# Kernel tuning notes

Measured on AMD Instinct MI355X. Metric: run time of the kernel, lower is better.

## Reference

```python
import jax, jax.numpy as jnp
import numpy as np


def _lstm_cell(x, h, c, Wih, Whh, bih, bhh):
    # torch.nn.LSTMCell: gates ordered (input, forget, cell, output)
    g = x @ Wih.T + h @ Whh.T + bih + bhh
    i, f, gg, o = jnp.split(g, 4, axis=-1)
    c2 = jax.nn.sigmoid(f) * c + jax.nn.sigmoid(i) * jnp.tanh(gg)
    h2 = jax.nn.sigmoid(o) * jnp.tanh(c2)
    return h2, c2


def setup_inputs() -> dict:
    key = jax.random.key(0)
    T, B, S, D = 64, 16, 128, 512
    ks = jax.random.split(key, 10)
    sc = 0.04  # ~ 1/sqrt(D) init scale
    z2 = jnp.zeros((B, D), jnp.float32)
    return {
        "emb_utts": jax.random.normal(ks[0], (T, B, D), jnp.float32),
        "M": jax.random.normal(ks[1], (B, S, D), jnp.float32),
        "hr0": z2, "cr0": z2, "hw0": z2, "cw0": z2,
        "Wih_r": jax.random.normal(ks[2], (4 * D, D), jnp.float32) * sc,
        "Whh_r": jax.random.normal(ks[3], (4 * D, D), jnp.float32) * sc,
        "bih_r": jnp.zeros((4 * D,), jnp.float32),
        "bhh_r": jnp.zeros((4 * D,), jnp.float32),
        "Wih_w": jax.random.normal(ks[4], (4 * D, D), jnp.float32) * sc,
        "Whh_w": jax.random.normal(ks[5], (4 * D, D), jnp.float32) * sc,
        "bih_w": jnp.zeros((4 * D,), jnp.float32),
        "bhh_w": jnp.zeros((4 * D,), jnp.float32),
        "Wc": jax.random.normal(ks[6], (D, 2 * D), jnp.float32) * sc,
        "bc": jnp.zeros((D,), jnp.float32),
    }


def reference(emb_utts, M, hr0, cr0, hw0, cw0,
              Wih_r, Whh_r, bih_r, bhh_r,
              Wih_w, Whh_w, bih_w, bhh_w, Wc, bc):
    def step(carry, w):
        hr, cr, hw, cw, Mc = carry
        # read LSTM (dropout is identity in eval)
        hr, cr = _lstm_cell(w, hr, cr, Wih_r, Whh_r, bih_r, bhh_r)
        # attention over memory
        sim = jnp.einsum('bd,bsd->bs', hr, Mc)
        z = jax.nn.softmax(sim, axis=-1)
        m = jnp.einsum('bs,bsd->bd', z, Mc)
        # compose + write LSTM
        comp = jnp.concatenate([hr, m], axis=-1) @ Wc.T + bc
        hw, cw = _lstm_cell(comp, hw, cw, Wih_w, Whh_w, bih_w, bhh_w)
        # memory update, faithful to source: M_new = (1 - z) * (M + hw)
        erase = 1.0 - z[:, :, None]
        Mc = erase * (Mc + hw[:, None, :])
        return (hr, cr, hw, cw, Mc), hw

    (hr, cr, hw, cw, Mf), outputs = jax.lax.scan(
        step, (hr0, cr0, hw0, cw0, M), emb_utts)
    return outputs, hr, cr, hw, cw, Mf
```

## Files before the change

kernel.cpp:

```cpp
#include <hip/hip_runtime.h>
#include <math.h>

#define TT 64
#define BB 16
#define SS 128
#define DD 512
#define NBLK 256
#define NTH 256
#define NSHARD 8
#define SHSTRIDE 64
#define BD (BB*DD)
#define OUT_HR   (TT*BD)
#define OUT_CR   (OUT_HR + BD)
#define OUT_HW   (OUT_CR + BD)
#define OUT_CW   (OUT_HW + BD)
#define OUT_MF   (OUT_CW + BD)
#define MAGIC 0x13579BDFu

#define HRR_OFF 0
#define HWR_OFF 532480
#define MR_OFF  1064960
#define SP_OFF  1589248
#define GE_OFF  1622016

#define OFF_WHR  0
#define OFF_WHW  4672
#define OFF_WFH  9344
#define OFF_WFM  14016
#define OFF_ABUF 18688
#define OFF_ML   28160
#define OFF_PRED 32256
#define OFF_GFB  36480
#define OFF_GFT  36608
#define OFF_ZL   36736
#define OFF_BFL  36992
#define OFF_SMW  37000
#define LDS_FLOATS 37008
#define LDS_BYTES  (LDS_FLOATS*4)
#define KH_W 292
#define KH_A 592

#define COLC(c) (((c) >> 1) * DD + dr0 + ((c) & 1))

__device__ __forceinline__ float sigf(float x) { return 1.f / (1.f + __expf(-x)); }

__device__ __forceinline__ void stg(float* p, float v) {
  __hip_atomic_store(p, v, __ATOMIC_RELAXED, __HIP_MEMORY_SCOPE_AGENT);
}
__device__ __forceinline__ float ldga(const float* p) {
  return __hip_atomic_load(p, __ATOMIC_RELAXED, __HIP_MEMORY_SCOPE_AGENT);
}

__device__ __forceinline__ void barrive(unsigned* cnt, unsigned& ep, int shard) {
  __syncthreads();
  if (threadIdx.x == 0) {
    ++ep;
    asm volatile("s_waitcnt vmcnt(0)" ::: "memory");
    __hip_atomic_fetch_add(cnt + shard * SHSTRIDE, 1u, __ATOMIC_RELAXED,
                           __HIP_MEMORY_SCOPE_AGENT);
  }
}
__device__ __forceinline__ void bwait(unsigned* cnt, unsigned ep) {
  if (threadIdx.x == 0) {
    const unsigned target = ep * (unsigned)NBLK;
    for (;;) {
      unsigned s = 0;
#pragma unroll
      for (int k = 0; k < NSHARD; ++k)
        s += __hip_atomic_load(cnt + k * SHSTRIDE, __ATOMIC_RELAXED,
                               __HIP_MEMORY_SCOPE_AGENT);
      if (s >= target) break;
      __builtin_amdgcn_s_sleep(1);
    }
  }
  __syncthreads();
}
__device__ __forceinline__ void lbar(unsigned* cnt, unsigned& ep, int shard) {
  barrive(cnt, ep, shard);
  bwait(cnt, ep);
}

__device__ __forceinline__ float dotf4(const float* __restrict__ a,
                                       const float* __restrict__ b, int n4) {
  const float4* a4 = (const float4*)a;
  const float4* b4 = (const float4*)b;
  float4 s = make_float4(0.f, 0.f, 0.f, 0.f);
#pragma unroll 8
  for (int k = 0; k < n4; ++k) {
    float4 x = a4[k], y = b4[k];
    s.x = fmaf(x.x, y.x, s.x); s.y = fmaf(x.y, y.y, s.y);
    s.z = fmaf(x.z, y.z, s.z); s.w = fmaf(x.w, y.w, s.w);
  }
  return (s.x + s.y) + (s.z + s.w);
}

__device__ __forceinline__ void dot_pass8(const float* __restrict__ A,
                                          const float* __restrict__ W,
                                          float* __restrict__ pout)
{
  float acc[8] = {0.f,0.f,0.f,0.f,0.f,0.f,0.f,0.f};
#pragma unroll
  for (int j = 0; j < 8; ++j) {
    float4 a4 = *(const float4*)(A + j*4);
#pragma unroll
    for (int c = 0; c < 8; ++c) {
      float4 w4 = *(const float4*)(W + c*36 + j*4);
      acc[c] = fmaf(a4.x, w4.x, acc[c]); acc[c] = fmaf(a4.y, w4.y, acc[c]);
      acc[c] = fmaf(a4.z, w4.z, acc[c]); acc[c] = fmaf(a4.w, w4.w, acc[c]);
    }
  }
  *(float4*)(pout)   = make_float4(acc[0],acc[1],acc[2],acc[3]);
  *(float4*)(pout+4) = make_float4(acc[4],acc[5],acc[6],acc[7]);
}

__device__ __forceinline__ void dot_pass8g(const float* __restrict__ ag,
                                           const float* __restrict__ Wb,
                                           int khq,
                                           float* __restrict__ pout)
{
  float acc[8] = {0.f,0.f,0.f,0.f,0.f,0.f,0.f,0.f};
#pragma unroll
  for (int jj = 0; jj < 2; ++jj) {
    const float* Wt = Wb + (khq*2 + jj)*KH_W;
#pragma unroll
    for (int j = 0; j < 8; ++j) {
      float4 a4 = *(const float4*)(ag + jj*32 + j*4);
#pragma unroll
      for (int c = 0; c < 8; ++c) {
        float4 w4 = *(const float4*)(Wt + c*36 + j*4);
        acc[c] = fmaf(a4.x, w4.x, acc[c]); acc[c] = fmaf(a4.y, w4.y, acc[c]);
        acc[c] = fmaf(a4.z, w4.z, acc[c]); acc[c] = fmaf(a4.w, w4.w, acc[c]);
      }
    }
  }
  *(float4*)(pout)   = make_float4(acc[0],acc[1],acc[2],acc[3]);
  *(float4*)(pout+4) = make_float4(acc[4],acc[5],acc[6],acc[7]);
}

__global__ void __launch_bounds__(NTH) memnet(
    const float* __restrict__ emb, const float* __restrict__ M_in,
    const float* __restrict__ hr0, const float* __restrict__ cr0,
    const float* __restrict__ hw0, const float* __restrict__ cw0,
    const float* __restrict__ Wih_r, const float* __restrict__ Whh_r,
    const float* __restrict__ bih_r, const float* __restrict__ bhh_r,
    const float* __restrict__ Wih_w, const float* __restrict__ Whh_w,
    const float* __restrict__ bih_w, const float* __restrict__ bhh_w,
    const float* __restrict__ Wc, const float* __restrict__ bc,
    float* __restrict__ out,
    unsigned* flagp, unsigned* cntp, float* __restrict__ wsf)
{
  extern __shared__ float L[];
  const int tid = threadIdx.x;
  const int bid = blockIdx.x;
  const int shard = bid & (NSHARD - 1);

  const int mb  = bid & 15;
  const int mdh = bid >> 4;
  const int dr0 = 2 * bid;

  float* hrr = wsf + HRR_OFF;
  float* hwr = wsf + HWR_OFF;
  float* mr  = wsf + MR_OFF;
  float* sp  = wsf + SP_OFF;
  float* gE  = wsf + GE_OFF + bid * (TT * 128);

  if (bid == 0) {
    if (tid == 0) {
#pragma unroll
      for (int k = 0; k < NSHARD; ++k)
        __hip_atomic_store(cntp + k * SHSTRIDE, 0u, __ATOMIC_RELAXED,
                           __HIP_MEMORY_SCOPE_AGENT);
      asm volatile("s_waitcnt vmcnt(0)" ::: "memory");
      __hip_atomic_store(flagp, MAGIC, __ATOMIC_RELAXED, __HIP_MEMORY_SCOPE_AGENT);
    }
  } else if (tid == 0) {
    while (__hip_atomic_load(flagp, __ATOMIC_RELAXED, __HIP_MEMORY_SCOPE_AGENT) != MAGIC) {}
  }
  __syncthreads();
  unsigned ep = 0;

  float cr = 0.f, cw = 0.f;
  if (tid >= 128 && tid < 160) {
    const int t = tid - 128, b = t & 15, dl = t >> 4;
    cr = cr0[b * DD + dr0 + dl];
    cw = cw0[b * DD + dr0 + dl];
  }

  {
    float* wih = L + OFF_ABUF;
#pragma unroll
    for (int c = 0; c < 8; ++c)
      ((float2*)(wih + c * DD))[tid] = ((const float2*)(Wih_w + COLC(c) * DD))[tid];
  }
  __syncthreads();
  {
    const float* wih = L + OFF_ABUF;
    float4 acc[8];
#pragma unroll
    for (int c = 0; c < 8; ++c) acc[c] = make_float4(0.f,0.f,0.f,0.f);
    const int k0 = tid * 4;
    for (int cc = 0; cc < DD; ++cc) {
      float4 wc4 = *(const float4*)(Wc + cc * 1024 + k0);
#pragma unroll
      for (int c = 0; c < 8; ++c) {
        const float wv = wih[c * DD + cc];
        acc[c].x = fmaf(wv, wc4.x, acc[c].x); acc[c].y = fmaf(wv, wc4.y, acc[c].y);
        acc[c].z = fmaf(wv, wc4.z, acc[c].z); acc[c].w = fmaf(wv, wc4.w, acc[c].w);
      }
    }
    const int kk = k0 & 511, kh = kk >> 5, jf = kk & 31;
    float* Tb = L + ((k0 < 512) ? OFF_WFH : OFF_WFM);
#pragma unroll
    for (int c = 0; c < 8; ++c)
      *(float4*)(Tb + kh*KH_W + c*36 + jf) = acc[c];
    if (tid < 8) {
      float s = 0.f;
      for (int cc = 0; cc < DD; ++cc) s = fmaf(wih[tid * DD + cc], bc[cc], s);
      L[OFF_BFL + tid] = s + bih_w[COLC(tid)] + bhh_w[COLC(tid)];
    }
  }
  __syncthreads();
  {
    const int c = tid >> 5, r = tid & 31;
    const int kk = r * 16, kh = kk >> 5, jb = (r & 1) * 16;
#pragma unroll
    for (int set = 0; set < 2; ++set) {
      const float* Wsrc = set ? Whh_w : Whh_r;
      float* dst = L + (set ? OFF_WHW : OFF_WHR) + kh*KH_W + c*36 + jb;
      const float* src = Wsrc + COLC(c) * DD + kk;
#pragma unroll
      for (int u = 0; u < 4; ++u)
        *(float4*)(dst + u*4) = *(const float4*)(src + u*4);
    }
  }
  {
    const int d_l = tid >> 3, sq = tid & 7;
    const int d = mdh * 32 + d_l;
#pragma unroll 4
    for (int j = 0; j < 16; ++j) {
      const int s = sq * 16 + j;
      L[OFF_ML + d_l * 128 + s] = M_in[(mb * SS + s) * DD + d];
    }
  }
  {
    const int tH = tid >> 7, b = (tid >> 3) & 15, c = tid & 7;
    const int col = COLC(c);
    const float bias = bih_r[col] + bhh_r[col];
    const float* wrow = Wih_r + col * DD;
    for (int t = tH * 32; t < tH * 32 + 32; ++t) {
      gE[t * 128 + b * 8 + c] = dotf4(emb + (t * BB + b) * DD, wrow, DD / 4) + bias;
    }
  }
  __syncthreads();
  {
#pragma unroll
    for (int j = 0; j < 8; ++j) {
      const int idx = j * 256 + tid;
      const int b = idx >> 7, k4 = idx & 127;
      const int kh = k4 >> 3, jf = (k4 & 7) * 4;
      float4 v = ((const float4*)hr0)[idx];
      *(float4*)(L + OFF_ABUF + kh*KH_A + b*36 + jf) = v;
    }
  }
  __syncthreads();
  {
    const int kh = tid >> 4, b = tid & 15;
    dot_pass8(L + OFF_ABUF + kh*KH_A + b*36, L + OFF_WHR + kh*KH_W,
              L + OFF_PRED + kh*132 + b*8);
  }
  __syncthreads();
  if (tid < 128) {
    float s = 0.f;
#pragma unroll
    for (int k2 = 0; k2 < 16; ++k2) s += L[OFF_PRED + k2*132 + tid];
    L[OFF_GFT + tid] = s;
  }
  __syncthreads();
  if (tid >= 128 && tid < 160) {
    const int t = tid - 128, b = t & 15, dl = t >> 4;
    float g[4];
#pragma unroll
    for (int q = 0; q < 4; ++q) {
      const int bc = b * 8 + q * 2 + dl;
      g[q] = L[OFF_GFT + bc] + gE[0 * 128 + bc];
    }
    cr = sigf(g[1]) * cr + sigf(g[0]) * tanhf(g[2]);
    const float h2 = sigf(g[3]) * tanhf(cr);
    stg(hrr + 1 * BD + b * DD + dr0 + dl, h2);
  }
  lbar(cntp, ep, shard);
  {
    const float* src = hrr + 1 * BD;
#pragma unroll
    for (int j = 0; j < 8; ++j) {
      const int idx = j * 256 + tid;
      const int b = idx >> 7, k4 = idx & 127;
      const int kh = k4 >> 3, jf = (k4 & 7) * 4;
      float4 v = ((const float4*)src)[idx];
      *(float4*)(L + OFF_ABUF + kh*KH_A + b*36 + jf) = v;
    }
  }
  __syncthreads();

  for (int i = 0; i < TT; ++i) {
    const int ii = i + 1;
    float* zold = L + OFF_ZL + ((i & 1) ^ 1) * 128;
    float* znew = L + OFF_ZL + (i & 1) * 128;

    {
      const int d_l = tid >> 3, sq = tid & 7;
      const float* Mrow = L + OFF_ML + d_l * 128;
      const float hrv = L[OFF_ABUF + mdh*KH_A + mb*36 + d_l];
#pragma unroll
      for (int j = 0; j < 4; ++j) {
        const int s4 = sq * 16 + j * 4;
        float4 M4 = *(const float4*)(Mrow + s4);
        float4 s;
        s.x = hrv * M4.x; s.y = hrv * M4.y; s.z = hrv * M4.z; s.w = hrv * M4.w;
        *(float4*)(L + OFF_PRED + d_l*132 + s4) = s;
      }
    }
    __syncthreads();
    if (tid < SS) {
      float v = 0.f;
#pragma unroll
      for (int dl2 = 0; dl2 < 32; ++dl2) v += L[OFF_PRED + dl2*132 + tid];
      stg(sp + (mb * 16 + mdh) * SS + tid, v);
    }
    barrive(cntp, ep, shard);

    if (ii < TT) {
      {
        const int kh = tid >> 4, b = tid & 15;
        dot_pass8(L + OFF_ABUF + kh*KH_A + b*36, L + OFF_WHR + kh*KH_W,
                  L + OFF_PRED + kh*132 + b*8);
      }
      __syncthreads();
      if (tid < 128) {
        float s = 0.f;
#pragma unroll
        for (int k2 = 0; k2 < 16; ++k2) s += L[OFF_PRED + k2*132 + tid];
        L[OFF_GFT + tid] = s;
      }
      __syncthreads();
      if (tid >= 128 && tid < 160) {
        const int t = tid - 128, b = t & 15, dl = t >> 4;
        float g[4];
#pragma unroll
        for (int q = 0; q < 4; ++q) {
          const int bc = b * 8 + q * 2 + dl;
          g[q] = L[OFF_GFT + bc] + gE[ii * 128 + bc];
        }
        cr = sigf(g[1]) * cr + sigf(g[0]) * tanhf(g[2]);
        const float h2 = sigf(g[3]) * tanhf(cr);
        stg(hrr + (ii + 1) * BD + b * DD + dr0 + dl, h2);
        if (ii == TT - 1) {
          out[OUT_HR + b * DD + dr0 + dl] = h2;
          out[OUT_CR + b * DD + dr0 + dl] = cr;
        }
      }
    }
    bwait(cntp, ep);

    float vsum = 0.f;
    if (tid < SS) {
#pragma unroll
      for (int j = 0; j < 16; ++j) vsum += ldga(sp + (mb * 16 + j) * SS + tid);
    } else if (i > 0) {
      const int t = tid - 128, k0 = t * 4;
      const float4 hw4 = *(const float4*)(hwr + i * BD + mb * DD + k0);
      const float4 a4  = *(const float4*)(L + OFF_ABUF + (k0 >> 5)*KH_A + mb*36 + (k0 & 31));
      float p = a4.x * hw4.x;
      p = fmaf(a4.y, hw4.y, p); p = fmaf(a4.z, hw4.z, p); p = fmaf(a4.w, hw4.w, p);
      for (int off = 32; off > 0; off >>= 1) p += __shfl_xor(p, off);
      if ((tid & 63) == 0) L[OFF_SMW + 6 + ((tid >> 6) & 1)] = p;
    }
    __syncthreads();
    if (tid < SS) {
      float v = vsum;
      if (i > 0) {
        const float hrdot = L[OFF_SMW + 6] + L[OFF_SMW + 7];
        v = (1.f - zold[tid]) * (v + hrdot);
      }
      float wm = v;
      for (int off = 32; off > 0; off >>= 1) wm = fmaxf(wm, __shfl_xor(wm, off));
      if ((tid & 63) == 0) L[OFF_SMW + (tid >> 6)] = wm;
      vsum = v;
    }
    __syncthreads();
    if (tid < SS) {
      const float gmax = fmaxf(L[OFF_SMW], L[OFF_SMW + 1]);
      const float e = __expf(vsum - gmax);
      float sm = e;
      for (int off = 32; off > 0; off >>= 1) sm += __shfl_xor(sm, off);
      if ((tid & 63) == 0) L[OFF_SMW + 2 + (tid >> 6)] = sm;
      vsum = e;
    }
    __syncthreads();
    if (tid < SS) znew[tid] = vsum / (L[OFF_SMW + 2] + L[OFF_SMW + 3]);
    __syncthreads();
    {
      const int d_l = tid >> 3, sq = tid & 7;
      float* Mrow = L + OFF_ML + d_l * 128;
      float mv = 0.f;
      if (i > 0) {
        const float hwv = hwr[i * BD + mb * DD + mdh * 32 + d_l];
#pragma unroll
        for (int j = 0; j < 4; ++j) {
          const int s4 = sq * 16 + j * 4;
          float4 M4  = *(float4*)(Mrow + s4);
          float4 zo4 = *(const float4*)(zold + s4);
          float4 zn4 = *(const float4*)(znew + s4);
          M4.x = (1.f - zo4.x) * (M4.x + hwv);
          M4.y = (1.f - zo4.y) * (M4.y + hwv);
          M4.z = (1.f - zo4.z) * (M4.z + hwv);
          M4.w = (1.f - zo4.w) * (M4.w + hwv);
          *(float4*)(Mrow + s4) = M4;
          mv = fmaf(zn4.x, M4.x, mv); mv = fmaf(zn4.y, M4.y, mv);
          mv = fmaf(zn4.z, M4.z, mv); mv = fmaf(zn4.w, M4.w, mv);
        }
      } else {
#pragma unroll
        for (int j = 0; j < 4; ++j) {
          const int s4 = sq * 16 + j * 4;
          float4 M4  = *(const float4*)(Mrow + s4);
          float4 zn4 = *(const float4*)(znew + s4);
          mv = fmaf(zn4.x, M4.x, mv); mv = fmaf(zn4.y, M4.y, mv);
          mv = fmaf(zn4.z, M4.z, mv); mv = fmaf(zn4.w, M4.w, mv);
        }
      }
      L[OFF_PRED + d_l * 8 + sq] = mv;
    }
    __syncthreads();
    if (tid < 32) {
      float mv = 0.f;
#pragma unroll
      for (int j = 0; j < 8; ++j) mv += L[OFF_PRED + tid * 8 + j];
      stg(mr + i * BD + mb * DD + mdh * 32 + tid, mv);
    }
    barrive(cntp, ep, shard);

    {
      const int kh = tid >> 4, b = tid & 15;
      dot_pass8(L + OFF_ABUF + kh*KH_A + b*36, L + OFF_WFH + kh*KH_W,
                L + OFF_PRED + 2112 + kh*132 + b*8);
    }
    bwait(cntp, ep);

    if (tid < 128) {
      float s = 0.f;
#pragma unroll
      for (int k2 = 0; k2 < 16; ++k2) s += L[OFF_PRED + 2112 + k2*132 + tid];
      L[OFF_GFB + tid] = s;
    }
    {
      const int src = tid >> 7, khq = (tid >> 4) & 7, b = tid & 15;
      const float* ag;
      const float* Wb;
      if (src == 0) { ag = mr + i * BD + b * DD + khq * 64; Wb = L + OFF_WFM; }
      else {
        const float* hwsrc = (i == 0) ? hw0 : (hwr + i * BD);
        ag = hwsrc + b * DD + khq * 64; Wb = L + OFF_WHW;
      }
      dot_pass8g(ag, Wb, khq, L + OFF_PRED + (src * 8 + khq) * 132 + b * 8);
    }
    __syncthreads();
    if (tid < 128) {
      float s = 0.f;
#pragma unroll
      for (int k2 = 0; k2 < 16; ++k2) s += L[OFF_PRED + k2*132 + tid];
      L[OFF_GFT + tid] = s;
    }
    __syncthreads();
    if (tid >= 128 && tid < 160) {
      const int t = tid - 128, b = t & 15, dl = t >> 4;
      float g[4];
#pragma unroll
      for (int q = 0; q < 4; ++q) {
        const int c = q * 2 + dl, bc = b * 8 + c;
        g[q] = L[OFF_GFB + bc] + L[OFF_GFT + bc] + L[OFF_BFL + c];
      }
      cw = sigf(g[1]) * cw + sigf(g[0]) * tanhf(g[2]);
      const float h2 = sigf(g[3]) * tanhf(cw);
      const int d = dr0 + dl;
      stg(hwr + (i + 1) * BD + b * DD + d, h2);
      out[i * BD + b * DD + d] = h2;
      if (i == TT - 1) {
        out[OUT_HW + b * DD + d] = h2;
        out[OUT_CW + b * DD + d] = cw;
      }
    }
    if (i < TT - 1) {
      const float* src = hrr + (i + 2) * BD;
#pragma unroll
      for (int j = 0; j < 8; ++j) {
        const int idx = j * 256 + tid;
        const int b = idx >> 7, k4 = idx & 127;
        const int kh = k4 >> 3, jf = (k4 & 7) * 4;
        float4 v = ((const float4*)src)[idx];
        *(float4*)(L + OFF_ABUF + kh*KH_A + b*36 + jf) = v;
      }
    }
    __syncthreads();
  }

  lbar(cntp, ep, shard);

  {
    const int d_l = tid >> 3, sq = tid & 7;
    const int d = mdh * 32 + d_l;
    const float hwv = hwr[TT * BD + mb * DD + d];
    const float* zfin = L + OFF_ZL + ((TT - 1) & 1) * 128;
#pragma unroll 4
    for (int j = 0; j < 16; ++j) {
      const int s = sq * 16 + j;
      const float nv = (1.f - zfin[s]) * (L[OFF_ML + d_l * 128 + s] + hwv);
      out[OUT_MF + (mb * SS + s) * DD + d] = nv;
    }
  }
}

extern "C" void kernel_launch(void* const* d_in, const int* in_sizes, int n_in,
                              void* d_out, int out_size, void* d_ws, size_t ws_size,
                              hipStream_t stream) {
  (void)in_sizes; (void)n_in; (void)out_size; (void)ws_size;
  const float* emb   = (const float*)d_in[0];
  const float* M_in  = (const float*)d_in[1];
  const float* hr0   = (const float*)d_in[2];
  const float* cr0   = (const float*)d_in[3];
  const float* hw0   = (const float*)d_in[4];
  const float* cw0   = (const float*)d_in[5];
  const float* Wih_r = (const float*)d_in[6];
  const float* Whh_r = (const float*)d_in[7];
  const float* bih_r = (const float*)d_in[8];
  const float* bhh_r = (const float*)d_in[9];
  const float* Wih_w = (const float*)d_in[10];
  const float* Whh_w = (const float*)d_in[11];
  const float* bih_w = (const float*)d_in[12];
  const float* bhh_w = (const float*)d_in[13];
  const float* Wc    = (const float*)d_in[14];
  const float* bc    = (const float*)d_in[15];
  float* out = (float*)d_out;

  char* wsb = (char*)d_ws;
  unsigned* flagp = (unsigned*)wsb;
  unsigned* cntp  = (unsigned*)(wsb + 1024);
  float* wsf = (float*)(wsb + 4096);

  static int attr_set = -1;
  (void)attr_set;
  hipFuncSetAttribute((const void*)memnet,
                      hipFuncAttributeMaxDynamicSharedMemorySize, LDS_BYTES);

  hipLaunchKernelGGL(memnet, dim3(NBLK), dim3(NTH), LDS_BYTES, stream,
                     emb, M_in, hr0, cr0, hw0, cw0,
                     Wih_r, Whh_r, bih_r, bhh_r,
                     Wih_w, Whh_w, bih_w, bhh_w, Wc, bc,
                     out, flagp, cntp, wsf);
}
```

Before: 1.418 ms.

## Replace polled sharded grid barrier with hierarchical counter and broadcast flags

Replaces the grid barrier, where each waiter polled and summed 8 shard counters, with a two-level counter tree. The last arriver in each of 32 shards bumps a master counter, and the final master arrival writes the epoch to 16 padded flag words, which each block polls as a single location. The GFB reduction is also moved ahead of the barrier wait so it overlaps with waiting. The aim is less polling traffic on contended lines and lower barrier latency, at the cost of a serial chain of extra atomics on the release path.

```diff
diff --git a/kernel.cpp b/kernel.cpp
--- a/kernel.cpp
+++ b/kernel.cpp
@@ -7,8 +7,6 @@
 #define DD 512
 #define NBLK 256
 #define NTH 256
-#define NSHARD 8
-#define SHSTRIDE 64
 #define BD (BB*DD)
 #define OUT_HR   (TT*BD)
 #define OUT_CR   (OUT_HR + BD)
@@ -16,6 +14,10 @@
 #define OUT_CW   (OUT_HW + BD)
 #define OUT_MF   (OUT_CW + BD)
 #define MAGIC 0x13579BDFu
+
+#define SY_MASTER 64
+#define SY_SHARD  256
+#define SY_FLAG   2048
 
 #define HRR_OFF 0
 #define HWR_OFF 532480
@@ -51,33 +53,38 @@
   return __hip_atomic_load(p, __ATOMIC_RELAXED, __HIP_MEMORY_SCOPE_AGENT);
 }
 
-__device__ __forceinline__ void barrive(unsigned* cnt, unsigned& ep, int shard) {
+__device__ __forceinline__ void barrive(unsigned* sync, unsigned& ep, int shard) {
   __syncthreads();
   if (threadIdx.x == 0) {
     ++ep;
     asm volatile("s_waitcnt vmcnt(0)" ::: "memory");
-    __hip_atomic_fetch_add(cnt + shard * SHSTRIDE, 1u, __ATOMIC_RELAXED,
-                           __HIP_MEMORY_SCOPE_AGENT);
-  }
-}
-__device__ __forceinline__ void bwait(unsigned* cnt, unsigned ep) {
+    unsigned o = __hip_atomic_fetch_add(sync + SY_SHARD + shard * 32, 1u,
+                                        __ATOMIC_RELAXED, __HIP_MEMORY_SCOPE_AGENT);
+    if ((o & 7u) == 7u) {
+      unsigned m = __hip_atomic_fetch_add(sync + SY_MASTER, 1u,
+                                          __ATOMIC_RELAXED, __HIP_MEMORY_SCOPE_AGENT);
+      if (((m + 1u) & 31u) == 0u) {
+        const unsigned done = (m + 1u) >> 5;
+#pragma unroll
+        for (int f = 0; f < 16; ++f)
+          __hip_atomic_store(sync + SY_FLAG + f * 32, done,
+                             __ATOMIC_RELAXED, __HIP_MEMORY_SCOPE_AGENT);
+      }
+    }
+  }
+}
+__device__ __forceinline__ void bwait(unsigned* sync, unsigned ep, int fl) {
   if (threadIdx.x == 0) {
-    const unsigned target = ep * (unsigned)NBLK;
-    for (;;) {
-      unsigned s = 0;
-#pragma unroll
-      for (int k = 0; k < NSHARD; ++k)
-        s += __hip_atomic_load(cnt + k * SHSTRIDE, __ATOMIC_RELAXED,
-                               __HIP_MEMORY_SCOPE_AGENT);
-      if (s >= target) break;
-      __builtin_amdgcn_s_sleep(1);
-    }
-  }
-  __syncthreads();
-}
-__device__ __forceinline__ void lbar(unsigned* cnt, unsigned& ep, int shard) {
-  barrive(cnt, ep, shard);
-  bwait(cnt, ep);
+    const unsigned* p = sync + SY_FLAG + fl * 32;
+    while (__hip_atomic_load(p, __ATOMIC_RELAXED, __HIP_MEMORY_SCOPE_AGENT) < ep) {
+      __builtin_amdgcn_s_sleep(2);
+    }
+  }
+  __syncthreads();
+}
+__device__ __forceinline__ void lbar(unsigned* sync, unsigned& ep, int shard, int fl) {
+  barrive(sync, ep, shard);
+  bwait(sync, ep, fl);
 }
 
 __device__ __forceinline__ float dotf4(const float* __restrict__ a,
@@ -147,12 +154,13 @@
     const float* __restrict__ bih_w, const float* __restrict__ bhh_w,
     const float* __restrict__ Wc, const float* __restrict__ bc,
     float* __restrict__ out,
-    unsigned* flagp, unsigned* cntp, float* __restrict__ wsf)
+    unsigned* sync, float* __restrict__ wsf)
 {
   extern __shared__ float L[];
   const int tid = threadIdx.x;
   const int bid = blockIdx.x;
-  const int shard = bid & (NSHARD - 1);
+  const int shard = bid & 31;
+  const int fl = bid & 15;
 
   const int mb  = bid & 15;
   const int mdh = bid >> 4;
@@ -166,15 +174,18 @@
 
   if (bid == 0) {
     if (tid == 0) {
-#pragma unroll
-      for (int k = 0; k < NSHARD; ++k)
-        __hip_atomic_store(cntp + k * SHSTRIDE, 0u, __ATOMIC_RELAXED,
-                           __HIP_MEMORY_SCOPE_AGENT);
+      __hip_atomic_store(sync + SY_MASTER, 0u, __ATOMIC_RELAXED, __HIP_MEMORY_SCOPE_AGENT);
+#pragma unroll
+      for (int k = 0; k < 32; ++k)
+        __hip_atomic_store(sync + SY_SHARD + k * 32, 0u, __ATOMIC_RELAXED, __HIP_MEMORY_SCOPE_AGENT);
+#pragma unroll
+      for (int f = 0; f < 16; ++f)
+        __hip_atomic_store(sync + SY_FLAG + f * 32, 0u, __ATOMIC_RELAXED, __HIP_MEMORY_SCOPE_AGENT);
       asm volatile("s_waitcnt vmcnt(0)" ::: "memory");
-      __hip_atomic_store(flagp, MAGIC, __ATOMIC_RELAXED, __HIP_MEMORY_SCOPE_AGENT);
+      __hip_atomic_store(sync, MAGIC, __ATOMIC_RELAXED, __HIP_MEMORY_SCOPE_AGENT);
     }
   } else if (tid == 0) {
-    while (__hip_atomic_load(flagp, __ATOMIC_RELAXED, __HIP_MEMORY_SCOPE_AGENT) != MAGIC) {}
+    while (__hip_atomic_load(sync, __ATOMIC_RELAXED, __HIP_MEMORY_SCOPE_AGENT) != MAGIC) {}
   }
   __syncthreads();
   unsigned ep = 0;
@@ -288,7 +299,7 @@
     const float h2 = sigf(g[3]) * tanhf(cr);
     stg(hrr + 1 * BD + b * DD + dr0 + dl, h2);
   }
-  lbar(cntp, ep, shard);
+  lbar(sync, ep, shard, fl);
   {
     const float* src = hrr + 1 * BD;
 #pragma unroll
@@ -327,7 +338,7 @@
       for (int dl2 = 0; dl2 < 32; ++dl2) v += L[OFF_PRED + dl2*132 + tid];
       stg(sp + (mb * 16 + mdh) * SS + tid, v);
     }
-    barrive(cntp, ep, shard);
+    barrive(sync, ep, shard);
 
     if (ii < TT) {
       {
@@ -360,7 +371,7 @@
         }
       }
     }
-    bwait(cntp, ep);
+    bwait(sync, ep, fl);
 
     float vsum = 0.f;
     if (tid < SS) {
@@ -438,21 +449,22 @@
       for (int j = 0; j < 8; ++j) mv += L[OFF_PRED + tid * 8 + j];
       stg(mr + i * BD + mb * DD + mdh * 32 + tid, mv);
     }
-    barrive(cntp, ep, shard);
+    barrive(sync, ep, shard);
 
     {
       const int kh = tid >> 4, b = tid & 15;
       dot_pass8(L + OFF_ABUF + kh*KH_A + b*36, L + OFF_WFH + kh*KH_W,
                 L + OFF_PRED + 2112 + kh*132 + b*8);
     }
-    bwait(cntp, ep);
-
+    __syncthreads();
     if (tid < 128) {
       float s = 0.f;
 #pragma unroll
       for (int k2 = 0; k2 < 16; ++k2) s += L[OFF_PRED + 2112 + k2*132 + tid];
       L[OFF_GFB + tid] = s;
     }
+    bwait(sync, ep, fl);
+
     {
       const int src = tid >> 7, khq = (tid >> 4) & 7, b = tid & 15;
       const float* ag;
@@ -504,7 +516,7 @@
     __syncthreads();
   }
 
-  lbar(cntp, ep, shard);
+  lbar(sync, ep, shard, fl);
 
   {
     const int d_l = tid >> 3, sq = tid & 7;
@@ -543,12 +555,9 @@
   float* out = (float*)d_out;
 
   char* wsb = (char*)d_ws;
-  unsigned* flagp = (unsigned*)wsb;
-  unsigned* cntp  = (unsigned*)(wsb + 1024);
-  float* wsf = (float*)(wsb + 4096);
-
-  static int attr_set = -1;
-  (void)attr_set;
+  unsigned* sync = (unsigned*)wsb;
+  float* wsf = (float*)(wsb + 16384);
+
   hipFuncSetAttribute((const void*)memnet,
                       hipFuncAttributeMaxDynamicSharedMemorySize, LDS_BYTES);
 
@@ -556,5 +565,5 @@
                      emb, M_in, hr0, cr0, hw0, cw0,
                      Wih_r, Whh_r, bih_r, bhh_r,
                      Wih_w, Whh_w, bih_w, bhh_w, Wc, bc,
-                     out, flagp, cntp, wsf);
-}
+                     out, sync, wsf);
+}
```

Result: slower. 1.565 ms (+10.3%).
